# Kernel tuning notes

Measured on AMD Instinct MI355X. Metric: run time of the kernel, lower is better.

Reference implementation:

```python
import jax, jax.numpy as jnp
import numpy as np

B, S, D = 2, 2048, 2048
H = 16
KV_RANK = 512
NOPE, ROPE = 128, 64
QK_HD = NOPE + ROPE  # 192
V_HD = 128
SCALE = QK_HD ** -0.5
EPS = 1.1920929e-07  # torch RMSNorm default eps = finfo(fp32).eps
NEG = -1e9


def rmsnorm(x, w):
    return x * jax.lax.rsqrt(jnp.mean(x * x, axis=-1, keepdims=True) + EPS) * w


def apply_rope(x, freqs):
    # x: (b, s, h, r) interleaved pairs; freqs: (s, r//2) angles
    sh = x.shape
    xr = x.reshape(*sh[:-1], -1, 2)
    a, b = xr[..., 0], xr[..., 1]
    cos = jnp.cos(freqs)[None, :, None, :]
    sin = jnp.sin(freqs)[None, :, None, :]
    return jnp.stack([a * cos - b * sin, a * sin + b * cos], axis=-1).reshape(sh)


def setup_inputs() -> dict:
    key = jax.random.key(0)
    ks = jax.random.split(key, 8)
    inv = lambda k, shape, fan_in: jax.random.uniform(k, shape, jnp.float32, -1.0, 1.0) / np.sqrt(fan_in)
    x = jax.random.normal(ks[0], (B, S, D), jnp.float32)
    freqs = jax.random.uniform(ks[1], (S, ROPE // 2), jnp.float32) * np.float32(np.pi)
    mask = jnp.where(jnp.triu(jnp.ones((S, S), bool), k=1), jnp.float32(NEG), jnp.float32(0.0))
    wq_w = inv(ks[2], (H * QK_HD, D), D)
    wq_b = jnp.zeros((H * QK_HD,), jnp.float32)
    wkv_a_w = inv(ks[3], (KV_RANK + ROPE, D), D)
    wkv_a_b = jnp.zeros((KV_RANK + ROPE,), jnp.float32)
    kv_norm_w = jnp.ones((KV_RANK,), jnp.float32)
    wkv_b_w = inv(ks[4], (H * (NOPE + V_HD), KV_RANK), KV_RANK)
    wo_w = inv(ks[5], (D, H * V_HD), H * V_HD)
    wo_b = jnp.zeros((D,), jnp.float32)
    return dict(x=x, freqs=freqs, mask=mask, wq_w=wq_w, wq_b=wq_b,
                wkv_a_w=wkv_a_w, wkv_a_b=wkv_a_b, kv_norm_w=kv_norm_w,
                wkv_b_w=wkv_b_w, wo_w=wo_w, wo_b=wo_b)


def reference(x, freqs, mask, wq_w, wq_b, wkv_a_w, wkv_a_b, kv_norm_w, wkv_b_w, wo_w, wo_b):
    b, s, _ = x.shape
    # q projection (q_lora_rank == 0 path)
    q = (x @ wq_w.T + wq_b).reshape(b, s, H, QK_HD)
    q_nope, q_pe = q[..., :NOPE], q[..., NOPE:]
    q_pe = apply_rope(q_pe, freqs)
    # latent kv projection
    kv = x @ wkv_a_w.T + wkv_a_b
    kv, k_pe = kv[..., :KV_RANK], kv[..., KV_RANK:]
    k_pe = apply_rope(k_pe[:, :, None, :], freqs)[:, :, 0, :]  # (b, t, r)
    kv_proj = rmsnorm(kv, kv_norm_w)  # (b, t, c)
    wkv_b = wkv_b_w.reshape(H, NOPE + V_HD, KV_RANK)
    # absorb K-nope projection into q
    q_nope = jnp.einsum('bshd,hdc->bshc', q_nope, wkv_b[:, :NOPE])
    scores = (jnp.einsum('bshc,btc->bsht', q_nope, kv_proj)
              + jnp.einsum('bshr,btr->bsht', q_pe, k_pe)) * SCALE
    scores = scores + mask[None, :, None, :]
    scores = jax.nn.softmax(scores.astype(jnp.float32), axis=-1).astype(x.dtype)
    out = jnp.einsum('bsht,btc->bshc', scores, kv_proj)
    out = jnp.einsum('bshc,hdc->bshd', out, wkv_b[:, -V_HD:])
    return out.reshape(b, s, H * V_HD) @ wo_w.T + wo_b
```

## Files before the change

### kernel.cpp

```cpp
#include <hip/hip_runtime.h>
#include <hip/hip_bf16.h>
#include <math.h>

#define B_ 2
#define S_ 2048
#define H_ 16
#define SCALE_ 0.07216878364870323f
#define SL2_ (0.07216878364870323f * 1.4426950408889634f)
#define EPS_ 1.1920929e-07f
#define M0_ 8.0f

typedef __attribute__((ext_vector_type(8))) short bf16x8;
typedef __attribute__((ext_vector_type(4))) float f32x4;
union U4 { uint4 u; bf16x8 v; f32x4 f; };

__device__ __forceinline__ uint bfbits(float x) {
    uint u = __float_as_uint(x);
    return (u + 0x7fffu + ((u >> 16) & 1u)) >> 16;
}
__device__ __forceinline__ uint pack2bf(float a, float b) {
    return bfbits(a) | (bfbits(b) << 16);
}
__device__ __forceinline__ uint cvtpk(float a, float b) {
    uint r;
    asm("v_cvt_pk_bf16_f32 %0, %1, %2" : "=v"(r) : "v"(a), "v"(b));
    return r;
}
__device__ __forceinline__ void gld_lds16(const ushort* g, ushort* l) {
    __builtin_amdgcn_global_load_lds(
        (const __attribute__((address_space(1))) uint*)g,
        (__attribute__((address_space(3))) uint*)l, 16, 0, 0);
}

template<int OM>
__global__ __launch_bounds__(256) void mgemm(
    const ushort* __restrict__ A, int lda, long long aOff1, long long aOff2,
    const ushort* __restrict__ Bm, int ldb, long long bOff1, long long bOff2,
    const float* __restrict__ bias, float scale,
    void* __restrict__ Cv, int ldc, long long cOff1, long long cOff2,
    int K, int zDiv, const float* __restrict__ freqs)
{
    __shared__ ushort As[2][128 * 32];
    __shared__ ushort Bs[2][128 * 32];

    const int z = blockIdx.z;
    const int z1 = z % zDiv, z2 = z / zDiv;
    A  += z1 * aOff1 + z2 * aOff2;
    Bm += z1 * bOff1 + z2 * bOff2;
    const long long cBase = z1 * cOff1 + z2 * cOff2;

    int bx = blockIdx.x, by = blockIdx.y;
    {
        const int gx = gridDim.x, total = gx * gridDim.y;
        if ((total & 7) == 0) {
            const int flat = bx + gx * by;
            const int nx = total >> 3;
            const int flat2 = (flat & 7) * nx + (flat >> 3);
            bx = flat2 % gx;
            by = flat2 / gx;
        }
    }
    const int n0 = bx * 128;
    const int m0 = by * 128;
    const int tid = threadIdx.x;
    const int w   = tid >> 6;
    const int l   = tid & 63;
    const int m   = l & 15;
    const int q4  = l >> 4;
    const int mw  = (w & 1) * 64;
    const int nw  = (w >> 1) * 64;
    const int sr  = l >> 2;
    const int sc  = l & 3;

    auto stageT = [&](int bi, int k0) {
#pragma unroll
        for (int jj = 0; jj < 2; ++jj) {
            const int slot = w * 2 + jj;
            const int row  = slot * 16 + sr;
            const int g    = sc ^ ((row >> 1) & 3);
            gld_lds16(&A[(long long)(m0 + row) * lda + k0 + g * 8], &As[bi][slot * 512]);
            gld_lds16(&Bm[(long long)(n0 + row) * ldb + k0 + g * 8], &Bs[bi][slot * 512]);
        }
    };

    f32x4 acc[4][4];
#pragma unroll
    for (int i = 0; i < 4; ++i)
#pragma unroll
        for (int j = 0; j < 4; ++j) acc[i][j] = (f32x4){0.f, 0.f, 0.f, 0.f};

    stageT(0, 0);
    int cur = 0;
    for (int k0 = 0; k0 < K; k0 += 32) {
        __syncthreads();
        if (k0 + 32 < K) stageT(cur ^ 1, k0 + 32);
        __builtin_amdgcn_sched_barrier(0);

        U4 af[4], bf[4];
#pragma unroll
        for (int i = 0; i < 4; ++i) {
            const int ra = mw + i * 16 + m;
            af[i].u = *(const uint4*)&As[cur][ra * 32 + (q4 ^ ((ra >> 1) & 3)) * 8];
            const int rb = nw + i * 16 + m;
            bf[i].u = *(const uint4*)&Bs[cur][rb * 32 + (q4 ^ ((rb >> 1) & 3)) * 8];
        }
#pragma unroll
        for (int i = 0; i < 4; ++i)
#pragma unroll
            for (int j = 0; j < 4; ++j)
                acc[i][j] = __builtin_amdgcn_mfma_f32_16x16x32_bf16(
                    af[i].v, bf[j].v, acc[i][j], 0, 0, 0);
        cur ^= 1;
    }

#pragma unroll
    for (int j = 0; j < 4; ++j) {
        const int cn = n0 + nw + j * 16 + m;
        const float bv = bias ? bias[cn] : 0.0f;
        const int d192 = cn % 192;
        const bool ropeW = (OM == 1) && (d192 >= 128);
        const int ri = (d192 - 128) >> 1;
        const bool evn = !(cn & 1);
#pragma unroll
        for (int i2 = 0; i2 < 4; ++i2) {
            const int rw = m0 + mw + i2 * 16 + q4 * 4;
#pragma unroll
            for (int r = 0; r < 4; ++r) {
                if (OM == 0) {
                    const float val = acc[i2][j][r] * scale + bv;
                    ((float*)Cv)[cBase + (long long)(rw + r) * ldc + cn] = val;
                } else if (OM == 1) {
                    float val = acc[i2][j][r] + bv;
                    if (ropeW) {
                        const float pv = __shfl_xor(val, 1, 64);
                        const float a  = evn ? val : pv;
                        const float b  = evn ? pv : val;
                        const int s = (rw + r) & 2047;
                        float cs, sn;
                        __sincosf(freqs[s * 32 + ri], &sn, &cs);
                        val = evn ? (a * cs - b * sn) : (a * sn + b * cs);
                    }
                    ((ushort*)Cv)[cBase + (long long)(rw + r) * ldc + cn] =
                        (ushort)bfbits(val * SL2_);
                } else if (OM == 2) {
                    const float val = acc[i2][j][r] * scale + bv;
                    const int t = rw + r, d = cn;
                    const long long idx =
                        ((((long long)(z2 * 64 + (t >> 5)) * 16 + z1) * 8
                          + (d >> 5) * 2 + ((t >> 4) & 1)) * 64
                         + ((d >> 3) & 3) * 16 + (t & 15)) * 8 + (d & 7);
                    ((ushort*)Cv)[idx] = (ushort)bfbits(val);
                } else {
                    const float val = acc[i2][j][r] * scale + bv;
                    const int d = rw + r, t = cn;
                    const long long idx =
                        ((((long long)(z2 * 64 + (t >> 5)) * 16 + z1) * 8
                          + (d >> 4)) * 64
                         + ((t >> 3) & 3) * 16 + (d & 15)) * 8 + (t & 7);
                    ((ushort*)Cv)[idx] = (ushort)bfbits(val);
                }
            }
        }
    }
}

__global__ __launch_bounds__(256) void conv_all(
    const float* __restrict__ x, const float* __restrict__ wq,
    const float* __restrict__ wkva, const float* __restrict__ wo,
    const float* __restrict__ wkvb,
    ushort* __restrict__ x_bf, ushort* __restrict__ wq_bf,
    ushort* __restrict__ wkva_bf, ushort* __restrict__ wo_bf,
    ushort* __restrict__ wkvbK, ushort* __restrict__ wkvbV)
{
    const int bid = blockIdx.x;
    const int tid = threadIdx.x;
    if (bid < 8192) {
        const long long i = ((long long)bid * 256 + tid) * 4;
        float4 v = *(const float4*)&x[i];
        uint2 p; p.x = pack2bf(v.x, v.y); p.y = pack2bf(v.z, v.w);
        *(uint2*)&x_bf[i] = p;
    } else if (bid < 14336) {
        const long long i = ((long long)(bid - 8192) * 256 + tid) * 4;
        float4 v = *(const float4*)&wq[i];
        uint2 p; p.x = pack2bf(v.x, v.y); p.y = pack2bf(v.z, v.w);
        *(uint2*)&wq_bf[i] = p;
    } else if (bid < 15616) {
        const int i = ((bid - 14336) * 256 + tid) * 4;
        const int r = i >> 11;
        uint2 p = make_uint2(0u, 0u);
        if (r < 576) {
            float4 v = *(const float4*)&wkva[i];
            p.x = pack2bf(v.x, v.y); p.y = pack2bf(v.z, v.w);
        }
        *(uint2*)&wkva_bf[i] = p;
    } else if (bid < 19712) {
        const long long i = ((long long)(bid - 15616) * 256 + tid) * 4;
        float4 v = *(const float4*)&wo[i];
        uint2 p; p.x = pack2bf(v.x, v.y); p.y = pack2bf(v.z, v.w);
        *(uint2*)&wo_bf[i] = p;
    } else if (bid < 20736) {
        const int i = ((bid - 19712) * 256 + tid) * 4;
        const int h = i >> 16, rem = i & 65535;
        float4 v = *(const float4*)&wkvb[((long long)(h * 256)) * 512 + rem];
        uint2 p; p.x = pack2bf(v.x, v.y); p.y = pack2bf(v.z, v.w);
        *(uint2*)&wkvbK[i] = p;
    } else {
        const int i = ((bid - 20736) * 256 + tid) * 4;
        const int h = i >> 16, rem = i & 65535;
        float4 v = *(const float4*)&wkvb[((long long)(h * 256 + 128)) * 512 + rem];
        uint2 p; p.x = pack2bf(v.x, v.y); p.y = pack2bf(v.z, v.w);
        *(uint2*)&wkvbV[i] = p;
    }
}

__global__ __launch_bounds__(64) void kv_post_kernel(
    const float* __restrict__ kv_raw, const float* __restrict__ bias,
    const float* __restrict__ w, const float* __restrict__ freqs,
    ushort* __restrict__ kv_h, uint* __restrict__ rimg)
{
    const int bs = blockIdx.x;
    const int lane = threadIdx.x;
    const float* src = kv_raw + (long long)bs * 640;
    ushort* dst = kv_h + (long long)bs * 576;

    const int c = 4 * lane;
    float4 v0 = *(const float4*)&src[c];
    float4 v1 = *(const float4*)&src[256 + c];
    float4 b0 = *(const float4*)&bias[c];
    float4 b1 = *(const float4*)&bias[256 + c];
    v0.x += b0.x; v0.y += b0.y; v0.z += b0.z; v0.w += b0.w;
    v1.x += b1.x; v1.y += b1.y; v1.z += b1.z; v1.w += b1.w;
    float ss = v0.x * v0.x + v0.y * v0.y + v0.z * v0.z + v0.w * v0.w +
               v1.x * v1.x + v1.y * v1.y + v1.z * v1.z + v1.w * v1.w;
#pragma unroll
    for (int o = 32; o; o >>= 1) ss += __shfl_xor(ss, o, 64);
    const float rs = rsqrtf(ss * (1.0f / 512.0f) + EPS_);

    float4 w0 = *(const float4*)&w[c];
    float4 w1 = *(const float4*)&w[256 + c];
    uint2 p0, p1;
    p0.x = pack2bf(v0.x * rs * w0.x, v0.y * rs * w0.y);
    p0.y = pack2bf(v0.z * rs * w0.z, v0.w * rs * w0.w);
    p1.x = pack2bf(v1.x * rs * w1.x, v1.y * rs * w1.y);
    p1.y = pack2bf(v1.z * rs * w1.z, v1.w * rs * w1.w);
    *(uint2*)&dst[c] = p0;
    *(uint2*)&dst[256 + c] = p1;

    if (lane < 32) {
        const int b = bs >> 11, s = bs & 2047;
        const int j = lane;
        const float f = freqs[s * 32 + j];
        float cs, sn;
        __sincosf(f, &sn, &cs);
        const float a  = src[512 + 2 * j]     + bias[512 + 2 * j];
        const float b2 = src[512 + 2 * j + 1] + bias[512 + 2 * j + 1];
        const uint p = pack2bf(a * cs - b2 * sn, a * sn + b2 * cs);
        const long long idx =
            (((long long)(b * 64 + (s >> 5)) * 4 + (j >> 4) * 2 + ((s >> 4) & 1)) * 64
             + ((j >> 2) & 3) * 16 + (s & 15)) * 4 + (j & 3);
        rimg[idx] = p;
    }
}

__global__ __launch_bounds__(256, 2) void attn_kernel(
    const ushort* __restrict__ q192,
    const uint4*  __restrict__ khimg,
    const uint4*  __restrict__ rimg,
    const uint4*  __restrict__ vhimg,
    float* __restrict__ part_o,
    float* __restrict__ part_l)
{
    __shared__ uint buf[2][20 * 256];

    const int hb   = blockIdx.x;
    const int h    = hb & 15;
    const int b    = hb >> 4;
    const int p    = blockIdx.y;
    const int par  = blockIdx.z;
    const int tid  = threadIdx.x;
    const int wid  = tid >> 6;
    const int lane = tid & 63;
    const int m    = lane & 15;
    const int q4   = lane >> 4;
    const bool odd = q4 & 1;

    auto stage = [&](int bs, int it) {
        const long long tb = (long long)(b * 64 + it);
        const uint4* kb = khimg + ((tb * 16 + h) * 8) * 64;
        const uint4* rb = rimg  + (tb * 4) * 64;
        const uint4* vb = vhimg + ((tb * 16 + h) * 8) * 64;
        ushort* l = (ushort*)&buf[bs][0];
        gld_lds16((const ushort*)(kb + (wid    ) * 64 + lane), l + (wid     ) * 512);
        gld_lds16((const ushort*)(kb + (wid + 4) * 64 + lane), l + (wid +  4) * 512);
        gld_lds16((const ushort*)(rb + (wid    ) * 64 + lane), l + (wid +  8) * 512);
        gld_lds16((const ushort*)(vb + (wid    ) * 64 + lane), l + (wid + 12) * 512);
        gld_lds16((const ushort*)(vb + (wid + 4) * 64 + lane), l + (wid + 16) * 512);
    };

    int cur = 0;
    for (int pass = 0; pass < 2; ++pass) {
        const int chunk = pass ? p : (15 - p);
        const int row0a = chunk * 128 + wid * 16;
        const int row0b = row0a + 64;
        const int sRa   = row0a + m;
        const int sRb   = row0b + m;

        U4 qfa[6], qfb[6];
        {
            const uint4* qpa = (const uint4*)(q192 + ((long long)(b * S_ + sRa) * H_ + h) * 192);
            const uint4* qpb = (const uint4*)(q192 + ((long long)(b * S_ + sRb) * H_ + h) * 192);
#pragma unroll
            for (int f = 0; f < 6; ++f) { qfa[f].u = qpa[f * 4 + q4]; qfb[f].u = qpb[f * 4 + q4]; }
        }

        f32x4 oA[8], oB[8];
#pragma unroll
        for (int c = 0; c < 8; ++c) {
            oA[c] = (f32x4){0.f, 0.f, 0.f, 0.f};
            oB[c] = (f32x4){0.f, 0.f, 0.f, 0.f};
        }
        float lA = 0.0f, lB = 0.0f;

        auto softpack = [&](const f32x4 s0, const f32x4 s1, int t0v, int rw0,
                            float& lac) -> U4 {
            float p00, p01, p02, p03, p10, p11, p12, p13;
            if (t0v + 31 <= rw0) {
                p00 = exp2f(s0[0] - M0_); p01 = exp2f(s0[1] - M0_);
                p02 = exp2f(s0[2] - M0_); p03 = exp2f(s0[3] - M0_);
                p10 = exp2f(s1[0] - M0_); p11 = exp2f(s1[1] - M0_);
                p12 = exp2f(s1[2] - M0_); p13 = exp2f(s1[3] - M0_);
            } else {
                const int sR = rw0 + m;
                const int tb0 = t0v + q4 * 4;
                const int tb1 = tb0 + 16;
                p00 = (tb0 + 0 <= sR) ? exp2f(s0[0] - M0_) : 0.0f;
                p01 = (tb0 + 1 <= sR) ? exp2f(s0[1] - M0_) : 0.0f;
                p02 = (tb0 + 2 <= sR) ? exp2f(s0[2] - M0_) : 0.0f;
                p03 = (tb0 + 3 <= sR) ? exp2f(s0[3] - M0_) : 0.0f;
                p10 = (tb1 + 0 <= sR) ? exp2f(s1[0] - M0_) : 0.0f;
                p11 = (tb1 + 1 <= sR) ? exp2f(s1[1] - M0_) : 0.0f;
                p12 = (tb1 + 2 <= sR) ? exp2f(s1[2] - M0_) : 0.0f;
                p13 = (tb1 + 3 <= sR) ? exp2f(s1[3] - M0_) : 0.0f;
            }
            lac += (p00 + p01) + (p02 + p03) + (p10 + p11) + (p12 + p13);
            uint X0 = cvtpk(p00, p01), X1 = cvtpk(p02, p03);
            uint Y0 = cvtpk(p10, p11), Y1 = cvtpk(p12, p13);
            asm("v_permlane32_swap_b32 %0, %1" : "+v"(X0), "+v"(Y0));
            asm("v_permlane32_swap_b32 %0, %1" : "+v"(X1), "+v"(Y1));
            uint u0 = odd ? X0 : Y0;
            uint u1 = odd ? X1 : Y1;
            uint w0 = (uint)__builtin_amdgcn_ds_swizzle((int)u0, 0x401F);
            uint w1 = (uint)__builtin_amdgcn_ds_swizzle((int)u1, 0x401F);
            U4 bb;
            bb.u.x = odd ? w0 : X0;
            bb.u.y = odd ? w1 : X1;
            bb.u.z = odd ? Y0 : w0;
            bb.u.w = odd ? Y1 : w1;
            return bb;
        };

        const int nT2 = 2 * chunk + 2;
        __syncthreads();
        stage(cur, par);

        for (int v = 0; v < nT2; ++v) {
            const int it = 2 * v + par;
            const int t0 = it * 32;
            __syncthreads();
            if (v + 1 < nT2) stage(cur ^ 1, it + 2);
            __builtin_amdgcn_sched_barrier(0);

            const uint* bb0 = &buf[cur][0];
            const int abase = lane * 4;
            const bool liveB = (t0 <= row0b + 15);
            const bool liveA = (t0 <= row0a + 15);
            const bool twoA  = (t0 < row0a);
            const bool twoB  = (t0 < row0b);

            if (liveB) {
                f32x4 sA0 = (f32x4){0.f,0.f,0.f,0.f}, sA1 = (f32x4){0.f,0.f,0.f,0.f};
                f32x4 sB0 = (f32x4){0.f,0.f,0.f,0.f}, sB1 = (f32x4){0.f,0.f,0.f,0.f};

                if (twoA) {
#pragma unroll
                    for (int f = 0; f < 6; ++f) {
                        const int ck = (f < 4) ? f * 2 : (f - 4) * 2 + 8;
                        U4 a0, a1;
                        a0.u = *(const uint4*)&bb0[ck * 256 + abase];
                        a1.u = *(const uint4*)&bb0[(ck + 1) * 256 + abase];
                        sA0 = __builtin_amdgcn_mfma_f32_16x16x32_bf16(a0.v, qfa[f].v, sA0, 0, 0, 0);
                        sB0 = __builtin_amdgcn_mfma_f32_16x16x32_bf16(a0.v, qfb[f].v, sB0, 0, 0, 0);
                        sA1 = __builtin_amdgcn_mfma_f32_16x16x32_bf16(a1.v, qfa[f].v, sA1, 0, 0, 0);
                        sB1 = __builtin_amdgcn_mfma_f32_16x16x32_bf16(a1.v, qfb[f].v, sB1, 0, 0, 0);
                    }
                } else {
#pragma unroll
                    for (int f = 0; f < 6; ++f) {
                        const int ck = (f < 4) ? f * 2 : (f - 4) * 2 + 8;
                        U4 a0;
                        a0.u = *(const uint4*)&bb0[ck * 256 + abase];
                        if (liveA)
                            sA0 = __builtin_amdgcn_mfma_f32_16x16x32_bf16(a0.v, qfa[f].v, sA0, 0, 0, 0);
                        sB0 = __builtin_amdgcn_mfma_f32_16x16x32_bf16(a0.v, qfb[f].v, sB0, 0, 0, 0);
                        if (twoB) {
                            U4 a1;
                            a1.u = *(const uint4*)&bb0[(ck + 1) * 256 + abase];
                            sB1 = __builtin_amdgcn_mfma_f32_16x16x32_bf16(a1.v, qfb[f].v, sB1, 0, 0, 0);
                        }
                    }
                }

                U4 bbB = softpack(sB0, sB1, t0, row0b, lB);
                if (liveA) {
                    U4 bbA = softpack(sA0, sA1, t0, row0a, lA);
#pragma unroll
                    for (int c = 0; c < 8; ++c) {
                        U4 av; av.u = *(const uint4*)&bb0[(12 + c) * 256 + abase];
                        oB[c] = __builtin_amdgcn_mfma_f32_16x16x32_bf16(av.v, bbB.v, oB[c], 0, 0, 0);
                        oA[c] = __builtin_amdgcn_mfma_f32_16x16x32_bf16(av.v, bbA.v, oA[c], 0, 0, 0);
                    }
                } else {
#pragma unroll
                    for (int c = 0; c < 8; ++c) {
                        U4 av; av.u = *(const uint4*)&bb0[(12 + c) * 256 + abase];
                        oB[c] = __builtin_amdgcn_mfma_f32_16x16x32_bf16(av.v, bbB.v, oB[c], 0, 0, 0);
                    }
                }
            }
            cur ^= 1;
        }

        lA += __shfl_xor(lA, 16, 64);
        lA += __shfl_xor(lA, 32, 64);
        lB += __shfl_xor(lB, 16, 64);
        lB += __shfl_xor(lB, 32, 64);

        const int cid  = (b * 16 + h) * 16 + chunk;
        const int slot = cid * 2 + par;
        float* po = part_o + (long long)slot * 16384;
        const int rA = wid * 16 + m;
        const int rB = rA + 64;
#pragma unroll
        for (int c = 0; c < 8; ++c) {
            *(f32x4*)&po[rA * 128 + c * 16 + q4 * 4] = oA[c];
            *(f32x4*)&po[rB * 128 + c * 16 + q4 * 4] = oB[c];
        }
        if (q4 == 0) {
            part_l[slot * 128 + rA] = lA;
            part_l[slot * 128 + rB] = lB;
        }
    }
}

__global__ __launch_bounds__(256) void combine_kernel(
    const float* __restrict__ part_o, const float* __restrict__ part_l,
    ushort* __restrict__ o_h)
{
    const int idx = blockIdx.x * 256 + threadIdx.x;
    const int d4  = (idx & 31) * 4;
    const int r   = (idx >> 5) & 127;
    const int cid = idx >> 12;
    const int chunk = cid & 15, h = (cid >> 4) & 15, b = cid >> 8;
    const long long s0 = (long long)(cid * 2) * 16384 + r * 128 + d4;
    float4 a = *(const float4*)&part_o[s0];
    float4 c = *(const float4*)&part_o[s0 + 16384];
    const float l = part_l[cid * 256 + r] + part_l[cid * 256 + 128 + r];
    const float inv = 1.0f / l;
    uint2 pk;
    pk.x = cvtpk((a.x + c.x) * inv, (a.y + c.y) * inv);
    pk.y = cvtpk((a.z + c.z) * inv, (a.w + c.w) * inv);
    const int s = chunk * 128 + r;
    *(uint2*)&o_h[(((long long)(b * S_ + s)) * H_ + h) * 128 + d4] = pk;
}

extern "C" void kernel_launch(void* const* d_in, const int* in_sizes, int n_in,
                              void* d_out, int out_size, void* d_ws, size_t ws_size,
                              hipStream_t stream)
{
    const float* x         = (const float*)d_in[0];
    const float* freqs     = (const float*)d_in[1];
    const float* wq_w      = (const float*)d_in[3];
    const float* wq_b      = (const float*)d_in[4];
    const float* wkv_a_w   = (const float*)d_in[5];
    const float* wkv_a_b   = (const float*)d_in[6];
    const float* kv_norm_w = (const float*)d_in[7];
    const float* wkv_b_w   = (const float*)d_in[8];
    const float* wo_w      = (const float*)d_in[9];
    const float* wo_b      = (const float*)d_in[10];
    float* out = (float*)d_out;

    char* w = (char*)d_ws;
    ushort* wo_bf   = (ushort*)w;  w += 8388608;
    uint4*  khimg   = (uint4*)w;   w += 16777216;
    uint4*  vhimg   = (uint4*)w;   w += 16777216;
    uint4*  rimg    = (uint4*)w;   w += 524288;
    ushort* q192    = (ushort*)w;  w += 25165824;
    ushort* o_h     = (ushort*)w;  w += 16777216;
    char* SCR = w;
    ushort* x_bf    = (ushort*)(SCR);
    ushort* wq_bf   = (ushort*)(SCR + 16777216);
    ushort* wkva_bf = (ushort*)(SCR + 29360128);
    ushort* wkvbK   = (ushort*)(SCR + 31981568);
    ushort* wkvbV   = (ushort*)(SCR + 34078720);
    float*  kv_raw  = (float*)(SCR + 36175872);
    ushort* kv_h    = (ushort*)(SCR);
    float*  part_o  = (float*)(SCR);
    float*  part_l  = (float*)(SCR + 67108864);

    dim3 blk(256);

    conv_all<<<dim3(21760), blk, 0, stream>>>(
        x, wq_w, wkv_a_w, wo_w, wkv_b_w,
        x_bf, wq_bf, wkva_bf, wo_bf, wkvbK, wkvbV);

    mgemm<1><<<dim3(24, 32, 1), blk, 0, stream>>>(
        x_bf, 2048, 0LL, 0LL, wq_bf, 2048, 0LL, 0LL, wq_b, 1.0f,
        q192, 3072, 0LL, 0LL, 2048, 1, freqs);

    mgemm<0><<<dim3(5, 32, 1), blk, 0, stream>>>(
        x_bf, 2048, 0LL, 0LL, wkva_bf, 2048, 0LL, 0LL, nullptr, 1.0f,
        kv_raw, 640, 0LL, 0LL, 2048, 1, nullptr);

    kv_post_kernel<<<dim3(4096), dim3(64), 0, stream>>>(
        kv_raw, wkv_a_b, kv_norm_w, freqs, kv_h, (uint*)rimg);

    mgemm<2><<<dim3(1, 16, 32), blk, 0, stream>>>(
        kv_h, 576, 0LL, (long long)S_ * 576,
        wkvbK, 512, 65536LL, 0LL, nullptr, 1.0f,
        khimg, 0, 0LL, 0LL, 512, 16, nullptr);
    mgemm<3><<<dim3(16, 1, 32), blk, 0, stream>>>(
        wkvbV, 512, 65536LL, 0LL,
        kv_h, 576, 0LL, (long long)S_ * 576, nullptr, 1.0f,
        vhimg, 0, 0LL, 0LL, 512, 16, nullptr);

    attn_kernel<<<dim3(32, 8, 2), blk, 0, stream>>>(
        q192, khimg, rimg, vhimg, part_o, part_l);

    combine_kernel<<<dim3(8192), blk, 0, stream>>>(part_o, part_l, o_h);

    mgemm<0><<<dim3(16, 32, 1), blk, 0, stream>>>(
        o_h, 2048, 0LL, 0LL, wo_bf, 2048, 0LL, 0LL, wo_b, 1.0f,
        out, 2048, 0LL, 0LL, 2048, 1, nullptr);
}
```

Before: 440.2 us.

## Fuse Q and latent-KV projections into one GEMM, drop LDS double buffering

The Q projection and the latent KV-A projection now run as a single GEMM launch over 3712 output columns. This works because the bf16 weight buffers are contiguous in scratch. Columns past 3072 are written as raw fp32 to the kv_raw buffer, and the rest get bias, RoPE and bf16 packing as before. Separately, the shared mgemm kernel drops its double-buffered LDS prefetch in favour of a single buffer with load, sync, compute, sync. That halves LDS use, which may raise occupancy, but it removes the overlap of global loads with MFMA work in every GEMM.

```diff
diff --git a/kernel.cpp b/kernel.cpp
--- a/kernel.cpp
+++ b/kernel.cpp
@@ -38,10 +38,10 @@
     const ushort* __restrict__ Bm, int ldb, long long bOff1, long long bOff2,
     const float* __restrict__ bias, float scale,
     void* __restrict__ Cv, int ldc, long long cOff1, long long cOff2,
-    int K, int zDiv, const float* __restrict__ freqs)
+    int K, int zDiv, const float* __restrict__ freqs, float* __restrict__ Cv2)
 {
-    __shared__ ushort As[2][128 * 32];
-    __shared__ ushort Bs[2][128 * 32];
+    __shared__ ushort As[128 * 32];
+    __shared__ ushort Bs[128 * 32];
 
     const int z = blockIdx.z;
     const int z1 = z % zDiv, z2 = z / zDiv;
@@ -72,37 +72,30 @@
     const int sr  = l >> 2;
     const int sc  = l & 3;
 
-    auto stageT = [&](int bi, int k0) {
+    f32x4 acc[4][4];
+#pragma unroll
+    for (int i = 0; i < 4; ++i)
+#pragma unroll
+        for (int j = 0; j < 4; ++j) acc[i][j] = (f32x4){0.f, 0.f, 0.f, 0.f};
+
+    for (int k0 = 0; k0 < K; k0 += 32) {
 #pragma unroll
         for (int jj = 0; jj < 2; ++jj) {
             const int slot = w * 2 + jj;
             const int row  = slot * 16 + sr;
             const int g    = sc ^ ((row >> 1) & 3);
-            gld_lds16(&A[(long long)(m0 + row) * lda + k0 + g * 8], &As[bi][slot * 512]);
-            gld_lds16(&Bm[(long long)(n0 + row) * ldb + k0 + g * 8], &Bs[bi][slot * 512]);
-        }
-    };
-
-    f32x4 acc[4][4];
-#pragma unroll
-    for (int i = 0; i < 4; ++i)
-#pragma unroll
-        for (int j = 0; j < 4; ++j) acc[i][j] = (f32x4){0.f, 0.f, 0.f, 0.f};
-
-    stageT(0, 0);
-    int cur = 0;
-    for (int k0 = 0; k0 < K; k0 += 32) {
+            gld_lds16(&A[(long long)(m0 + row) * lda + k0 + g * 8], &As[slot * 512]);
+            gld_lds16(&Bm[(long long)(n0 + row) * ldb + k0 + g * 8], &Bs[slot * 512]);
+        }
         __syncthreads();
-        if (k0 + 32 < K) stageT(cur ^ 1, k0 + 32);
-        __builtin_amdgcn_sched_barrier(0);
 
         U4 af[4], bf[4];
 #pragma unroll
         for (int i = 0; i < 4; ++i) {
             const int ra = mw + i * 16 + m;
-            af[i].u = *(const uint4*)&As[cur][ra * 32 + (q4 ^ ((ra >> 1) & 3)) * 8];
+            af[i].u = *(const uint4*)&As[ra * 32 + (q4 ^ ((ra >> 1) & 3)) * 8];
             const int rb = nw + i * 16 + m;
-            bf[i].u = *(const uint4*)&Bs[cur][rb * 32 + (q4 ^ ((rb >> 1) & 3)) * 8];
+            bf[i].u = *(const uint4*)&Bs[rb * 32 + (q4 ^ ((rb >> 1) & 3)) * 8];
         }
 #pragma unroll
         for (int i = 0; i < 4; ++i)
@@ -110,15 +103,16 @@
             for (int j = 0; j < 4; ++j)
                 acc[i][j] = __builtin_amdgcn_mfma_f32_16x16x32_bf16(
                     af[i].v, bf[j].v, acc[i][j], 0, 0, 0);
-        cur ^= 1;
+        __syncthreads();
     }
 
 #pragma unroll
     for (int j = 0; j < 4; ++j) {
         const int cn = n0 + nw + j * 16 + m;
-        const float bv = bias ? bias[cn] : 0.0f;
+        const bool kvReg = (OM == 4) && (cn >= 3072);
+        const float bv = (bias && !kvReg) ? bias[cn] : 0.0f;
         const int d192 = cn % 192;
-        const bool ropeW = (OM == 1) && (d192 >= 128);
+        const bool ropeW = (OM == 4) && !kvReg && (d192 >= 128);
         const int ri = (d192 - 128) >> 1;
         const bool evn = !(cn & 1);
 #pragma unroll
@@ -129,19 +123,24 @@
                 if (OM == 0) {
                     const float val = acc[i2][j][r] * scale + bv;
                     ((float*)Cv)[cBase + (long long)(rw + r) * ldc + cn] = val;
-                } else if (OM == 1) {
-                    float val = acc[i2][j][r] + bv;
-                    if (ropeW) {
-                        const float pv = __shfl_xor(val, 1, 64);
-                        const float a  = evn ? val : pv;
-                        const float b  = evn ? pv : val;
-                        const int s = (rw + r) & 2047;
-                        float cs, sn;
-                        __sincosf(freqs[s * 32 + ri], &sn, &cs);
-                        val = evn ? (a * cs - b * sn) : (a * sn + b * cs);
+                } else if (OM == 4) {
+                    if (kvReg) {
+                        ((float*)Cv2)[(long long)(rw + r) * 640 + (cn - 3072)] =
+                            acc[i2][j][r];
+                    } else {
+                        float val = acc[i2][j][r] + bv;
+                        if (ropeW) {
+                            const float pv = __shfl_xor(val, 1, 64);
+                            const float a  = evn ? val : pv;
+                            const float b  = evn ? pv : val;
+                            const int s = (rw + r) & 2047;
+                            float cs, sn;
+                            __sincosf(freqs[s * 32 + ri], &sn, &cs);
+                            val = evn ? (a * cs - b * sn) : (a * sn + b * cs);
+                        }
+                        ((ushort*)Cv)[(long long)(rw + r) * 3072 + cn] =
+                            (ushort)bfbits(val * SL2_);
                     }
-                    ((ushort*)Cv)[cBase + (long long)(rw + r) * ldc + cn] =
-                        (ushort)bfbits(val * SL2_);
                 } else if (OM == 2) {
                     const float val = acc[i2][j][r] * scale + bv;
                     const int t = rw + r, d = cn;
@@ -513,13 +512,9 @@
         x, wq_w, wkv_a_w, wo_w, wkv_b_w,
         x_bf, wq_bf, wkva_bf, wo_bf, wkvbK, wkvbV);
 
-    mgemm<1><<<dim3(24, 32, 1), blk, 0, stream>>>(
+    mgemm<4><<<dim3(29, 32, 1), blk, 0, stream>>>(
         x_bf, 2048, 0LL, 0LL, wq_bf, 2048, 0LL, 0LL, wq_b, 1.0f,
-        q192, 3072, 0LL, 0LL, 2048, 1, freqs);
-
-    mgemm<0><<<dim3(5, 32, 1), blk, 0, stream>>>(
-        x_bf, 2048, 0LL, 0LL, wkva_bf, 2048, 0LL, 0LL, nullptr, 1.0f,
-        kv_raw, 640, 0LL, 0LL, 2048, 1, nullptr);
+        q192, 3072, 0LL, 0LL, 2048, 1, freqs, kv_raw);
 
     kv_post_kernel<<<dim3(4096), dim3(64), 0, stream>>>(
         kv_raw, wkv_a_b, kv_norm_w, freqs, kv_h, (uint*)rimg);
@@ -527,11 +522,11 @@
     mgemm<2><<<dim3(1, 16, 32), blk, 0, stream>>>(
         kv_h, 576, 0LL, (long long)S_ * 576,
         wkvbK, 512, 65536LL, 0LL, nullptr, 1.0f,
-        khimg, 0, 0LL, 0LL, 512, 16, nullptr);
+        khimg, 0, 0LL, 0LL, 512, 16, nullptr, nullptr);
     mgemm<3><<<dim3(16, 1, 32), blk, 0, stream>>>(
         wkvbV, 512, 65536LL, 0LL,
         kv_h, 576, 0LL, (long long)S_ * 576, nullptr, 1.0f,
-        vhimg, 0, 0LL, 0LL, 512, 16, nullptr);
+        vhimg, 0, 0LL, 0LL, 512, 16, nullptr, nullptr);
 
     attn_kernel<<<dim3(32, 8, 2), blk, 0, stream>>>(
         q192, khimg, rimg, vhimg, part_o, part_l);
@@ -540,5 +535,5 @@
 
     mgemm<0><<<dim3(16, 32, 1), blk, 0, stream>>>(
         o_h, 2048, 0LL, 0LL, wo_bf, 2048, 0LL, 0LL, wo_b, 1.0f,
-        out, 2048, 0LL, 0LL, 2048, 1, nullptr);
-}
+        out, 2048, 0LL, 0LL, 2048, 1, nullptr, nullptr);
+}
```

New measurement: 466.3 us. +5.9%, slower.
